# Kernel tuning notes

Hardware: AMD Instinct MI355X
Metric: run time of the kernel (lower is better)

## Reference

```python
import jax, jax.numpy as jnp
from jax import lax
import numpy as np
import math

DIM = 96      # channels
HEADS = 3     # num_heads
WS = 8        # window size
SHIFT = 4     # window_size // 2 (depth is odd -> shifted)
TLC = 64      # tlc_kernel
H = 264
W = 264


def _grid_idxes(h, w, k1, k2):
    # Faithful replication of the torch grids() tiling index logic (static ints).
    num_row = (h - 1) // k1 + 1
    num_col = (w - 1) // k2 + 1
    step_j = k2 if num_col == 1 else math.ceil((w - k2) / (num_col - 1) - 1e-8)
    step_i = k1 if num_row == 1 else math.ceil((h - k1) / (num_row - 1) - 1e-8)
    idxes = []
    i = 0
    last_i = False
    while i < h and not last_i:
        j = 0
        if i + k1 >= h:
            i = h - k1
            last_i = True
        last_j = False
        while j < w and not last_j:
            if j + k2 >= w:
                j = w - k2
                last_j = True
            idxes.append((i, j))
            j = j + step_j
        i = i + step_i
    return idxes


def setup_inputs() -> dict:
    key = jax.random.key(0)
    ks = jax.random.split(key, 4)
    return {
        "x": jax.random.normal(ks[0], (1, DIM, H, W), jnp.float32),
        "temperature": jnp.ones((HEADS, 1, 1), jnp.float32),
        "qkv_w": jax.random.normal(ks[1], (3 * DIM, DIM), jnp.float32) * 0.05,
        "dw_w": jax.random.normal(ks[2], (3 * DIM, 1, 3, 3), jnp.float32) * 0.1,
        "proj_w": jax.random.normal(ks[3], (DIM, DIM), jnp.float32) * 0.05,
    }


def reference(x, temperature, qkv_w, dw_w, proj_w):
    b, c, h, w = x.shape
    # depth % 2 == 1 -> cyclic shift
    x = jnp.roll(x, (-SHIFT, -SHIFT), axis=(2, 3))
    # 1x1 pointwise conv (no bias)
    qkv = jnp.einsum('oc,bchw->bohw', qkv_w, x)
    # 3x3 depthwise conv, padding 1
    qkv = lax.conv_general_dilated(
        qkv, dw_w, window_strides=(1, 1), padding=[(1, 1), (1, 1)],
        feature_group_count=3 * c, dimension_numbers=('NCHW', 'OIHW', 'NCHW'))
    # --- TLC grids: overlapping tiles (eval path, b == 1) ---
    k1, k2 = min(h, TLC), min(w, TLC)
    idxes = _grid_idxes(h, w, k1, k2)
    parts = jnp.concatenate([qkv[:, :, i:i + k1, j:j + k2] for (i, j) in idxes], axis=0)  # [T,3c,k1,k2]
    T, C3, th, tw = parts.shape
    nh, nw = th // WS, tw // WS
    # window partition: b c (h b0) (w b1) -> (b h w) c b0 b1 -> flatten spatial
    win = parts.reshape(T, C3, nh, WS, nw, WS).transpose(0, 2, 4, 1, 3, 5)
    win = win.reshape(T * nh * nw, C3, WS * WS)  # [Bw, 3c, 64]
    q, k, v = jnp.split(win, 3, axis=1)  # each [Bw, c, 64]
    ch = c // HEADS
    q = q.reshape(-1, HEADS, ch, WS * WS)
    k = k.reshape(-1, HEADS, ch, WS * WS)
    v = v.reshape(-1, HEADS, ch, WS * WS)
    # L2 normalize along token dim (F.normalize eps=1e-12)
    q = q / jnp.maximum(jnp.linalg.norm(q, axis=-1, keepdims=True), 1e-12)
    k = k / jnp.maximum(jnp.linalg.norm(k, axis=-1, keepdims=True), 1e-12)
    # channel attention: [Bw, head, ch, ch]
    attn = jax.nn.relu(jnp.einsum('bhcn,bhdn->bhcd', q, k) * temperature)
    out = jnp.einsum('bhcd,bhdn->bhcn', attn, v)  # [Bw, head, ch, 64]
    out = out.reshape(-1, c, WS, WS)
    # window merge back to tiles
    out = out.reshape(T, nh, nw, c, WS, WS).transpose(0, 3, 1, 4, 2, 5).reshape(T, c, th, tw)
    # --- TLC grids_inverse: scatter-add overlapping tiles and average ---
    preds = jnp.zeros((b, c, h, w), x.dtype)
    cnt = np.zeros((h, w), np.float32)
    for t, (i, j) in enumerate(idxes):
        preds = preds.at[0, :, i:i + k1, j:j + k2].add(out[t])
        cnt[i:i + k1, j:j + k2] += 1.0
    preds = preds / jnp.asarray(cnt)
    # 1x1 output projection
    out = jnp.einsum('oc,bchw->bohw', proj_w, preds)
    # undo cyclic shift
    return jnp.roll(out, (SHIFT, SHIFT), axis=(2, 3))
```

## Files before the change

### kernel.cpp

```cpp
#include <hip/hip_runtime.h>
#include <hip/hip_bf16.h>

#define HW_ 69696
#define W_ 264
#define H_ 264

typedef short bf16x8 __attribute__((ext_vector_type(8)));
typedef float f32x4 __attribute__((ext_vector_type(4)));

static __device__ __forceinline__ unsigned short f2b(float f) {
  __hip_bfloat16 h = __float2bfloat16(f);
  return *reinterpret_cast<unsigned short*>(&h);
}
static __device__ __forceinline__ float b2f(unsigned short u) {
  __hip_bfloat16 h;
  *reinterpret_cast<unsigned short*>(&h) = u;
  return __bfloat162float(h);
}
static __device__ __forceinline__ float lo_f(unsigned int u) {
  union { unsigned int i; float f; } c; c.i = u << 16; return c.f;
}
static __device__ __forceinline__ float hi_f(unsigned int u) {
  union { unsigned int i; float f; } c; c.i = u & 0xffff0000u; return c.f;
}

__global__ __launch_bounds__(256) void k_pre(const float* __restrict__ x,
                                             unsigned short* __restrict__ xbT) {
  __shared__ unsigned short t_[96 * 70];
  __shared__ int rp[64];
  const int tid = threadIdx.x;
  const int px0 = blockIdx.x * 64;
  if (tid < 64) {
    int p = px0 + tid;
    int y = p / W_, xx = p - y * W_;
    int y2 = y + 4; if (y2 >= H_) y2 -= H_;
    int x2 = xx + 4; if (x2 >= W_) x2 -= W_;
    rp[tid] = y2 * W_ + x2;
  }
  __syncthreads();
  for (int l = tid; l < 96 * 64; l += 256) {
    int c = l >> 6, j = l & 63;
    t_[c * 70 + j] = f2b(x[c * HW_ + rp[j]]);
  }
  __syncthreads();
  const int pxl = tid >> 2, qp = tid & 3;
  unsigned int tmp[12];
#pragma unroll
  for (int i = 0; i < 12; ++i) {
    unsigned int lo = t_[(qp * 24 + 2 * i) * 70 + pxl];
    unsigned int hi = t_[(qp * 24 + 2 * i + 1) * 70 + pxl];
    tmp[i] = lo | (hi << 16);
  }
  uint4* dst = (uint4*)(xbT + (size_t)(px0 + pxl) * 96 + qp * 24);
  dst[0] = make_uint4(tmp[0], tmp[1], tmp[2], tmp[3]);
  dst[1] = make_uint4(tmp[4], tmp[5], tmp[6], tmp[7]);
  dst[2] = make_uint4(tmp[8], tmp[9], tmp[10], tmp[11]);
}

__global__ __launch_bounds__(256, 3) void k_gemm(const float* __restrict__ w,
                                                 const unsigned short* __restrict__ bT,
                                                 unsigned short* __restrict__ outb) {
  __shared__ __align__(16) char smem[46592];
  unsigned short* As = (unsigned short*)smem;
  unsigned short* Bs = As + 96 * 104;

  const int tid = threadIdx.x;
  const int px0 = blockIdx.x * 128;
  const int oc = blockIdx.y;
  const int npx = min(128, HW_ - px0);

  const float* wp = w + oc * 96 * 96;
  for (int l = tid; l < 96 * 24; l += 256) {
    int o = l / 24, c4 = (l - (l / 24) * 24) * 4;
    float4 v = *(const float4*)&wp[o * 96 + c4];
    unsigned int p0 = (unsigned int)f2b(v.x) | ((unsigned int)f2b(v.y) << 16);
    unsigned int p1 = (unsigned int)f2b(v.z) | ((unsigned int)f2b(v.w) << 16);
    *(uint2*)&As[o * 104 + c4] = make_uint2(p0, p1);
  }
  {
    const int nbytes = npx * 192;
    const char* src = (const char*)(bT + (size_t)px0 * 96);
    for (int off = tid * 16; off < nbytes; off += 256 * 16) {
      uint4 v = *(const uint4*)(src + off);
      int row = off / 192;
      int colb = off - row * 192;
      *(uint4*)((char*)Bs + row * 208 + colb) = v;
    }
  }
  __syncthreads();

  const int wid = tid >> 6, lane = tid & 63;
  const int quad = lane >> 4, lo = lane & 15;
  f32x4 acc[6][2];
#pragma unroll
  for (int mt = 0; mt < 6; ++mt)
#pragma unroll
    for (int nt = 0; nt < 2; ++nt) acc[mt][nt] = {0.f, 0.f, 0.f, 0.f};

#pragma unroll
  for (int ks = 0; ks < 3; ++ks) {
    const int kb = ks * 32 + quad * 8;
    bf16x8 b[2];
#pragma unroll
    for (int nt = 0; nt < 2; ++nt)
      b[nt] = *(const bf16x8*)&Bs[(wid * 32 + nt * 16 + lo) * 104 + kb];
#pragma unroll
    for (int mt = 0; mt < 6; ++mt) {
      bf16x8 a = *(const bf16x8*)&As[(mt * 16 + lo) * 104 + kb];
#pragma unroll
      for (int nt = 0; nt < 2; ++nt)
        acc[mt][nt] = __builtin_amdgcn_mfma_f32_16x16x32_bf16(a, b[nt], acc[mt][nt], 0, 0, 0);
    }
  }

  __syncthreads();
  unsigned short* Cs2 = (unsigned short*)smem;
#pragma unroll
  for (int mt = 0; mt < 6; ++mt)
#pragma unroll
    for (int nt = 0; nt < 2; ++nt) {
      int px_l = wid * 32 + nt * 16 + lo;
#pragma unroll
      for (int r = 0; r < 4; ++r)
        Cs2[px_l * 104 + mt * 16 + quad * 4 + r] = f2b(acc[mt][nt][r]);
    }
  __syncthreads();
  for (int i = tid; i < 128 * 12; i += 256) {
    int pxl = i & 127, j = i >> 7;
    if (px0 + pxl < HW_)
      *((uint4*)outb + (size_t)(oc * 12 + j) * HW_ + px0 + pxl) =
          ((const uint4*)(Cs2 + pxl * 104))[j];
  }
}

__global__ __launch_bounds__(256) void k_dw(const unsigned short* __restrict__ qkv,
                                            const float* __restrict__ dw,
                                            unsigned short* __restrict__ out) {
  __shared__ __align__(16) uint4 inS[18 * 66];
  const int tid = threadIdx.x;
  const int x0 = blockIdx.x * 64;
  const int y0 = blockIdx.y * 16;
  const int u = blockIdx.z;
  const uint4* plane = (const uint4*)qkv + (size_t)u * HW_;
  const float* wp = dw + u * 72;
  float wv[72];
#pragma unroll
  for (int i = 0; i < 72; ++i) wv[i] = wp[i];

  for (int idx = tid; idx < 18 * 66; idx += 256) {
    int rr = idx / 66, cc = idx - rr * 66;
    int gy = y0 - 1 + rr, gx = x0 - 1 + cc;
    uint4 v = make_uint4(0u, 0u, 0u, 0u);
    if ((unsigned)gy < (unsigned)H_ && (unsigned)gx < (unsigned)W_)
      v = plane[gy * W_ + gx];
    inS[idx] = v;
  }
  __syncthreads();

#pragma unroll
  for (int k = 0; k < 4; ++k) {
    const int oidx = k * 256 + tid;
    const int ro = oidx >> 6, co = oidx & 63;
    const int y = y0 + ro, x = x0 + co;
    float acc[8] = {0.f, 0.f, 0.f, 0.f, 0.f, 0.f, 0.f, 0.f};
#pragma unroll
    for (int dy = 0; dy < 3; ++dy)
#pragma unroll
      for (int dx = 0; dx < 3; ++dx) {
        uint4 v = inS[(ro + dy) * 66 + co + dx];
        float w0 = wv[0 * 9 + dy * 3 + dx], w1 = wv[1 * 9 + dy * 3 + dx];
        float w2 = wv[2 * 9 + dy * 3 + dx], w3 = wv[3 * 9 + dy * 3 + dx];
        float w4 = wv[4 * 9 + dy * 3 + dx], w5 = wv[5 * 9 + dy * 3 + dx];
        float w6 = wv[6 * 9 + dy * 3 + dx], w7 = wv[7 * 9 + dy * 3 + dx];
        acc[0] += w0 * lo_f(v.x); acc[1] += w1 * hi_f(v.x);
        acc[2] += w2 * lo_f(v.y); acc[3] += w3 * hi_f(v.y);
        acc[4] += w4 * lo_f(v.z); acc[5] += w5 * hi_f(v.z);
        acc[6] += w6 * lo_f(v.w); acc[7] += w7 * hi_f(v.w);
      }
    if (y < H_ && x < W_) {
      uint4 o;
      o.x = (unsigned int)f2b(acc[0]) | ((unsigned int)f2b(acc[1]) << 16);
      o.y = (unsigned int)f2b(acc[2]) | ((unsigned int)f2b(acc[3]) << 16);
      o.z = (unsigned int)f2b(acc[4]) | ((unsigned int)f2b(acc[5]) << 16);
      o.w = (unsigned int)f2b(acc[6]) | ((unsigned int)f2b(acc[7]) << 16);
      *((uint4*)out + (size_t)u * HW_ + y * W_ + x) = o;
    }
  }
}

#define P1 296
#define P8 2376
__global__ __launch_bounds__(192) void k_attn(const unsigned short* __restrict__ qd,
                                              const float* __restrict__ temp,
                                              unsigned short* __restrict__ tout) {
  __shared__ __align__(16) unsigned short flat[8 * P8];
  __shared__ __align__(16) unsigned short attnL[3 * 32 * 40];
  __shared__ float invn[3 * 32];
  const int tid = threadIdx.x;
  const int wi = blockIdx.x, t = blockIdx.y;
  const int i0 = (t / 5) * 50, j0 = (t % 5) * 50;
  const int wy = wi >> 3, wx = wi & 7;
  const int gy0 = i0 + wy * 8, gx0 = j0 + wx * 8;

  {
    const size_t base = (size_t)gy0 * W_ + gx0;
    for (int idx = tid; idx < 36 * 64; idx += 192) {
      int u = idx >> 6, rj = idx & 63, r = rj >> 3, j = rj & 7;
      uint4 v = ((const uint4*)qd)[(size_t)u * HW_ + base + r * W_ + j];
      ((uint4*)flat)[r * 297 + j * 37 + u] = v;
    }
  }
  __syncthreads();

  const int h = tid >> 6, lane = tid & 63;
  const int quad = lane >> 4, lo = lane & 15;
  const int cb = h * 32;

  bf16x8 qf[2][2], kf[2][2];
#pragma unroll
  for (int mt = 0; mt < 2; ++mt)
#pragma unroll
    for (int kt = 0; kt < 2; ++kt) {
      const int rbase = (kt * 4 + quad) * P8;
      const int cq = cb + mt * 16 + lo;
      const int ck = 96 + cb + mt * 16 + lo;
      bf16x8 q8, k8;
#pragma unroll
      for (int j = 0; j < 8; ++j) {
        q8[j] = (short)flat[rbase + j * P1 + cq];
        k8[j] = (short)flat[rbase + j * P1 + ck];
      }
      qf[mt][kt] = q8;
      kf[mt][kt] = k8;
    }

  f32x4 S[2][2];
#pragma unroll
  for (int mt = 0; mt < 2; ++mt)
#pragma unroll
    for (int nt = 0; nt < 2; ++nt) {
      S[mt][nt] = {0.f, 0.f, 0.f, 0.f};
#pragma unroll
      for (int kt = 0; kt < 2; ++kt)
        S[mt][nt] = __builtin_amdgcn_mfma_f32_16x16x32_bf16(qf[mt][kt], kf[nt][kt], S[mt][nt], 0, 0, 0);
    }

  float ivk[2];
#pragma unroll
  for (int mt = 0; mt < 2; ++mt) {
    float sq = 0.f, sk = 0.f;
#pragma unroll
    for (int kt = 0; kt < 2; ++kt)
#pragma unroll
      for (int j = 0; j < 8; ++j) {
        float a = b2f((unsigned short)qf[mt][kt][j]);
        float b = b2f((unsigned short)kf[mt][kt][j]);
        sq += a * a;
        sk += b * b;
      }
    sq += __shfl_xor(sq, 16);
    sq += __shfl_xor(sq, 32);
    sk += __shfl_xor(sk, 16);
    sk += __shfl_xor(sk, 32);
    if (quad == 0) invn[h * 32 + mt * 16 + lo] = 1.f / fmaxf(sqrtf(sq), 1e-12f);
    ivk[mt] = 1.f / fmaxf(sqrtf(sk), 1e-12f);
  }
  __syncthreads();

  const float ts = temp[h];
#pragma unroll
  for (int mt = 0; mt < 2; ++mt)
#pragma unroll
    for (int nt = 0; nt < 2; ++nt)
#pragma unroll
      for (int r = 0; r < 4; ++r) {
        int c = mt * 16 + quad * 4 + r;
        float v = S[mt][nt][r] * invn[h * 32 + c] * ivk[nt] * ts;
        attnL[(h * 32 + c) * 40 + nt * 16 + lo] = f2b(fmaxf(v, 0.f));
      }
  __syncthreads();

  bf16x8 af[2];
#pragma unroll
  for (int mt = 0; mt < 2; ++mt)
    af[mt] = *(const bf16x8*)&attnL[(h * 32 + mt * 16 + lo) * 40 + quad * 8];

  f32x4 O[2][4];
#pragma unroll
  for (int nt = 0; nt < 4; ++nt) {
    const int px = nt * 16 + lo;
    bf16x8 vf = *(const bf16x8*)&flat[(px >> 3) * P8 + (px & 7) * P1 + 192 + cb + quad * 8];
#pragma unroll
    for (int mt = 0; mt < 2; ++mt) {
      f32x4 z = {0.f, 0.f, 0.f, 0.f};
      O[mt][nt] = __builtin_amdgcn_mfma_f32_16x16x32_bf16(af[mt], vf, z, 0, 0, 0);
    }
  }
  __syncthreads();

  unsigned short* Cs = flat;
#pragma unroll
  for (int mt = 0; mt < 2; ++mt)
#pragma unroll
    for (int nt = 0; nt < 4; ++nt) {
      const int px = nt * 16 + lo;
      unsigned int p0 = (unsigned int)f2b(O[mt][nt][0]) | ((unsigned int)f2b(O[mt][nt][1]) << 16);
      unsigned int p1 = (unsigned int)f2b(O[mt][nt][2]) | ((unsigned int)f2b(O[mt][nt][3]) << 16);
      *(uint2*)&Cs[px * 104 + cb + mt * 16 + quad * 4] = make_uint2(p0, p1);
    }
  __syncthreads();

  for (int idx = tid; idx < 64 * 12; idx += 192) {
    int rec = idx / 12, u = idx - (idx / 12) * 12;
    int r = rec >> 3, j = rec & 7;
    size_t g = (size_t)t * 4096 + (wy * 8 + r) * 64 + wx * 8 + j;
    ((uint4*)tout)[g * 12 + u] = ((const uint4*)(Cs + rec * 104))[u];
  }
}

__global__ __launch_bounds__(256, 4) void k_avgproj(const float* __restrict__ w,
                                                    const unsigned short* __restrict__ tout,
                                                    float* __restrict__ outf) {
  __shared__ __align__(16) char smem[33280];
  unsigned short* As = (unsigned short*)smem;
  unsigned short* Bs = As + 96 * 104;

  const int tid = threadIdx.x;
  const int px0 = blockIdx.x * 64;

  for (int l = tid; l < 96 * 24; l += 256) {
    int o = l / 24, c4 = (l - (l / 24) * 24) * 4;
    float4 v = *(const float4*)&w[o * 96 + c4];
    unsigned int p0 = (unsigned int)f2b(v.x) | ((unsigned int)f2b(v.y) << 16);
    unsigned int p1 = (unsigned int)f2b(v.z) | ((unsigned int)f2b(v.w) << 16);
    *(uint2*)&As[o * 104 + c4] = make_uint2(p0, p1);
  }

  {
    const int pxl = tid >> 2, q = tid & 3;
    const int px = px0 + pxl;
    unsigned short* bd = Bs + pxl * 104 + q * 24;
    const int y = px / W_, xx = px - y * W_;
    int loy = (y >= 64) ? (y - 14) / 50 : 0;
    int hiy = y / 50; if (hiy > 4) hiy = 4;
    int lox = (xx >= 64) ? (xx - 14) / 50 : 0;
    int hix = xx / 50; if (hix > 4) hix = 4;
    float acc[24];
#pragma unroll
    for (int i = 0; i < 24; ++i) acc[i] = 0.f;
    int cnt = 0;
    for (int ty = loy; ty <= hiy; ++ty)
      for (int tx = lox; tx <= hix; ++tx) {
        size_t rec = (size_t)(ty * 5 + tx) * 4096 + ((y - ty * 50) << 6) + (xx - tx * 50);
        const uint4* rp = (const uint4*)tout + rec * 12 + q * 3;
#pragma unroll
        for (int ui = 0; ui < 3; ++ui) {
          uint4 v = rp[ui];
          acc[ui * 8 + 0] += lo_f(v.x); acc[ui * 8 + 1] += hi_f(v.x);
          acc[ui * 8 + 2] += lo_f(v.y); acc[ui * 8 + 3] += hi_f(v.y);
          acc[ui * 8 + 4] += lo_f(v.z); acc[ui * 8 + 5] += hi_f(v.z);
          acc[ui * 8 + 6] += lo_f(v.w); acc[ui * 8 + 7] += hi_f(v.w);
        }
        ++cnt;
      }
    const float inv = 1.f / (float)cnt;
#pragma unroll
    for (int ui = 0; ui < 3; ++ui) {
      uint4 o;
      o.x = (unsigned int)f2b(acc[ui * 8 + 0] * inv) | ((unsigned int)f2b(acc[ui * 8 + 1] * inv) << 16);
      o.y = (unsigned int)f2b(acc[ui * 8 + 2] * inv) | ((unsigned int)f2b(acc[ui * 8 + 3] * inv) << 16);
      o.z = (unsigned int)f2b(acc[ui * 8 + 4] * inv) | ((unsigned int)f2b(acc[ui * 8 + 5] * inv) << 16);
      o.w = (unsigned int)f2b(acc[ui * 8 + 6] * inv) | ((unsigned int)f2b(acc[ui * 8 + 7] * inv) << 16);
      ((uint4*)bd)[ui] = o;
    }
  }
  __syncthreads();

  const int wid = tid >> 6, lane = tid & 63;
  const int quad = lane >> 4, lo = lane & 15;
  f32x4 acc[6];
#pragma unroll
  for (int mt = 0; mt < 6; ++mt) acc[mt] = {0.f, 0.f, 0.f, 0.f};

#pragma unroll
  for (int ks = 0; ks < 3; ++ks) {
    const int kb = ks * 32 + quad * 8;
    bf16x8 b = *(const bf16x8*)&Bs[(wid * 16 + lo) * 104 + kb];
#pragma unroll
    for (int mt = 0; mt < 6; ++mt) {
      bf16x8 a = *(const bf16x8*)&As[(mt * 16 + lo) * 104 + kb];
      acc[mt] = __builtin_amdgcn_mfma_f32_16x16x32_bf16(a, b, acc[mt], 0, 0, 0);
    }
  }

  {
    int px = px0 + wid * 16 + lo;
    int y = px / W_, xx = px - y * W_;
    int y2 = y + 4; if (y2 >= H_) y2 -= H_;
    int x2 = xx + 4; if (x2 >= W_) x2 -= W_;
    int tp = y2 * W_ + x2;
#pragma unroll
    for (int mt = 0; mt < 6; ++mt) {
      int row = mt * 16 + quad * 4;
#pragma unroll
      for (int r = 0; r < 4; ++r)
        outf[(size_t)(row + r) * HW_ + tp] = acc[mt][r];
    }
  }
}

extern "C" void kernel_launch(void* const* d_in, const int* in_sizes, int n_in,
                              void* d_out, int out_size, void* d_ws, size_t ws_size,
                              hipStream_t stream) {
  (void)in_sizes; (void)n_in; (void)out_size; (void)ws_size;
  const float* x = (const float*)d_in[0];
  const float* temp = (const float*)d_in[1];
  const float* qkvw = (const float*)d_in[2];
  const float* dww = (const float*)d_in[3];
  const float* projw = (const float*)d_in[4];
  float* out = (float*)d_out;

  char* ws = (char*)d_ws;
  const size_t SZQ = (size_t)288 * HW_ * 2;
  unsigned short* qkvb = (unsigned short*)ws;
  unsigned short* tout = (unsigned short*)ws;
  unsigned short* xbT = (unsigned short*)(ws + SZQ);
  unsigned short* qkvd = (unsigned short*)(ws + SZQ);

  k_pre<<<dim3(1089), 256, 0, stream>>>(x, xbT);
  k_gemm<<<dim3(545, 3), 256, 0, stream>>>(qkvw, xbT, qkvb);
  k_dw<<<dim3(5, 17, 36), 256, 0, stream>>>(qkvb, dww, qkvd);
  k_attn<<<dim3(64, 25), 192, 0, stream>>>(qkvd, temp, tout);
  k_avgproj<<<dim3(1089), 256, 0, stream>>>(projw, tout, out);
}
```

Baseline: 172.5 us.

## Fuse shift/transpose prepass into QKV GEMM and load V directly in attention

Removes the separate k_pre kernel: the GEMM now computes rolled pixel indices itself and gathers fp32 x for 8 channels at a time, converting to bf16 while filling its B tile in shared memory. This drops one launch and a bf16 intermediate round-trip, but each of the 3 output-channel blocks now re-reads and re-converts the fp32 input. In k_attn only Q and K are staged into shared memory (24 instead of 36 units), with the shared-memory pitch reduced to match. V fragments are now read straight from global memory per MFMA tile, cutting shared memory use at the cost of strided global loads.

```diff
diff --git a/kernel.cpp b/kernel.cpp
--- a/kernel.cpp
+++ b/kernel.cpp
@@ -24,50 +24,29 @@
   union { unsigned int i; float f; } c; c.i = u & 0xffff0000u; return c.f;
 }
 
-__global__ __launch_bounds__(256) void k_pre(const float* __restrict__ x,
-                                             unsigned short* __restrict__ xbT) {
-  __shared__ unsigned short t_[96 * 70];
-  __shared__ int rp[64];
-  const int tid = threadIdx.x;
-  const int px0 = blockIdx.x * 64;
-  if (tid < 64) {
-    int p = px0 + tid;
-    int y = p / W_, xx = p - y * W_;
-    int y2 = y + 4; if (y2 >= H_) y2 -= H_;
-    int x2 = xx + 4; if (x2 >= W_) x2 -= W_;
-    rp[tid] = y2 * W_ + x2;
-  }
-  __syncthreads();
-  for (int l = tid; l < 96 * 64; l += 256) {
-    int c = l >> 6, j = l & 63;
-    t_[c * 70 + j] = f2b(x[c * HW_ + rp[j]]);
-  }
-  __syncthreads();
-  const int pxl = tid >> 2, qp = tid & 3;
-  unsigned int tmp[12];
-#pragma unroll
-  for (int i = 0; i < 12; ++i) {
-    unsigned int lo = t_[(qp * 24 + 2 * i) * 70 + pxl];
-    unsigned int hi = t_[(qp * 24 + 2 * i + 1) * 70 + pxl];
-    tmp[i] = lo | (hi << 16);
-  }
-  uint4* dst = (uint4*)(xbT + (size_t)(px0 + pxl) * 96 + qp * 24);
-  dst[0] = make_uint4(tmp[0], tmp[1], tmp[2], tmp[3]);
-  dst[1] = make_uint4(tmp[4], tmp[5], tmp[6], tmp[7]);
-  dst[2] = make_uint4(tmp[8], tmp[9], tmp[10], tmp[11]);
-}
-
-__global__ __launch_bounds__(256, 3) void k_gemm(const float* __restrict__ w,
-                                                 const unsigned short* __restrict__ bT,
+__global__ __launch_bounds__(256, 3) void k_gemm(const float* __restrict__ x,
+                                                 const float* __restrict__ w,
                                                  unsigned short* __restrict__ outb) {
   __shared__ __align__(16) char smem[46592];
+  __shared__ int rp[128];
   unsigned short* As = (unsigned short*)smem;
   unsigned short* Bs = As + 96 * 104;
 
   const int tid = threadIdx.x;
   const int px0 = blockIdx.x * 128;
   const int oc = blockIdx.y;
-  const int npx = min(128, HW_ - px0);
+
+  if (tid < 128) {
+    int p = px0 + tid;
+    int r = 0;
+    if (p < HW_) {
+      int y = p / W_, xx = p - y * W_;
+      int y2 = y + 4; if (y2 >= H_) y2 -= H_;
+      int x2 = xx + 4; if (x2 >= W_) x2 -= W_;
+      r = y2 * W_ + x2;
+    }
+    rp[tid] = r;
+  }
 
   const float* wp = w + oc * 96 * 96;
   for (int l = tid; l < 96 * 24; l += 256) {
@@ -77,15 +56,28 @@
     unsigned int p1 = (unsigned int)f2b(v.z) | ((unsigned int)f2b(v.w) << 16);
     *(uint2*)&As[o * 104 + c4] = make_uint2(p0, p1);
   }
-  {
-    const int nbytes = npx * 192;
-    const char* src = (const char*)(bT + (size_t)px0 * 96);
-    for (int off = tid * 16; off < nbytes; off += 256 * 16) {
-      uint4 v = *(const uint4*)(src + off);
-      int row = off / 192;
-      int colb = off - row * 192;
-      *(uint4*)((char*)Bs + row * 208 + colb) = v;
-    }
+  __syncthreads();
+
+  for (int l = tid; l < 128 * 12; l += 256) {
+    int pxl = l & 127, g = l >> 7;
+    uint4 o = make_uint4(0u, 0u, 0u, 0u);
+    if (px0 + pxl < HW_) {
+      const int base = rp[pxl];
+      const float* xp = x + (size_t)(g * 8) * HW_ + base;
+      float f0 = xp[0];
+      float f1 = xp[HW_];
+      float f2 = xp[2 * HW_];
+      float f3 = xp[3 * HW_];
+      float f4 = xp[4 * HW_];
+      float f5 = xp[5 * HW_];
+      float f6 = xp[6 * HW_];
+      float f7 = xp[7 * HW_];
+      o.x = (unsigned int)f2b(f0) | ((unsigned int)f2b(f1) << 16);
+      o.y = (unsigned int)f2b(f2) | ((unsigned int)f2b(f3) << 16);
+      o.z = (unsigned int)f2b(f4) | ((unsigned int)f2b(f5) << 16);
+      o.w = (unsigned int)f2b(f6) | ((unsigned int)f2b(f7) << 16);
+    }
+    *(uint4*)&Bs[pxl * 104 + g * 8] = o;
   }
   __syncthreads();
 
@@ -188,8 +180,8 @@
   }
 }
 
-#define P1 296
-#define P8 2376
+#define P1 200
+#define P8 1608
 __global__ __launch_bounds__(192) void k_attn(const unsigned short* __restrict__ qd,
                                               const float* __restrict__ temp,
                                               unsigned short* __restrict__ tout) {
@@ -204,10 +196,10 @@
 
   {
     const size_t base = (size_t)gy0 * W_ + gx0;
-    for (int idx = tid; idx < 36 * 64; idx += 192) {
+    for (int idx = tid; idx < 24 * 64; idx += 192) {
       int u = idx >> 6, rj = idx & 63, r = rj >> 3, j = rj & 7;
       uint4 v = ((const uint4*)qd)[(size_t)u * HW_ + base + r * W_ + j];
-      ((uint4*)flat)[r * 297 + j * 37 + u] = v;
+      ((uint4*)flat)[r * 201 + j * 25 + u] = v;
     }
   }
   __syncthreads();
@@ -285,11 +277,14 @@
   for (int mt = 0; mt < 2; ++mt)
     af[mt] = *(const bf16x8*)&attnL[(h * 32 + mt * 16 + lo) * 40 + quad * 8];
 
+  const int uv = 24 + h * 4 + quad;
   f32x4 O[2][4];
 #pragma unroll
   for (int nt = 0; nt < 4; ++nt) {
     const int px = nt * 16 + lo;
-    bf16x8 vf = *(const bf16x8*)&flat[(px >> 3) * P8 + (px & 7) * P1 + 192 + cb + quad * 8];
+    const size_t gpx = (size_t)(gy0 + (px >> 3)) * W_ + gx0 + (px & 7);
+    uint4 vraw = ((const uint4*)qd)[(size_t)uv * HW_ + gpx];
+    bf16x8 vf = *reinterpret_cast<bf16x8*>(&vraw);
 #pragma unroll
     for (int mt = 0; mt < 2; ++mt) {
       f32x4 z = {0.f, 0.f, 0.f, 0.f};
@@ -424,11 +419,9 @@
   const size_t SZQ = (size_t)288 * HW_ * 2;
   unsigned short* qkvb = (unsigned short*)ws;
   unsigned short* tout = (unsigned short*)ws;
-  unsigned short* xbT = (unsigned short*)(ws + SZQ);
   unsigned short* qkvd = (unsigned short*)(ws + SZQ);
 
-  k_pre<<<dim3(1089), 256, 0, stream>>>(x, xbT);
-  k_gemm<<<dim3(545, 3), 256, 0, stream>>>(qkvw, xbT, qkvb);
+  k_gemm<<<dim3(545, 3), 256, 0, stream>>>(x, qkvw, qkvb);
   k_dw<<<dim3(5, 17, 36), 256, 0, stream>>>(qkvb, dww, qkvd);
   k_attn<<<dim3(64, 25), 192, 0, stream>>>(qkvd, temp, tout);
   k_avgproj<<<dim3(1089), 256, 0, stream>>>(projw, tout, out);
```

After: 163.4 us. 1.06x faster.
